# Optimization experiments

Measured on AMD Instinct MI355X. Metric: run time of the kernel, lower is better.

The kernel has to match this reference:

```python
import jax, jax.numpy as jnp
import numpy as np

B, S, D, H = 16, 512, 1024, 16
DH = D // H  # 64


def setup_inputs() -> dict:
    key = jax.random.key(0)
    kx, kq, kk, kv = jax.random.split(key, 4)
    stdv = 1.0 / np.sqrt(DH)  # reset_param uses 1/sqrt(t.size(1)) = 1/sqrt(head_dim)
    x = jax.random.normal(kx, (B, S, D), dtype=jnp.float32)
    Wq = jax.random.uniform(kq, (H, D, DH), dtype=jnp.float32, minval=-stdv, maxval=stdv)
    Wk = jax.random.uniform(kk, (H, D, DH), dtype=jnp.float32, minval=-stdv, maxval=stdv)
    Wv = jax.random.uniform(kv, (H, D, DH), dtype=jnp.float32, minval=-stdv, maxval=stdv)
    return {"x": x, "Wq": Wq, "Wk": Wk, "Wv": Wv}


def reference(x, Wq, Wk, Wv):
    # x: [B, S, D]; Wq/Wk/Wv: [H, D, DH] (stacked per-head params)
    q = jnp.einsum('bsd,hde->bhse', x, Wq)  # [B,H,S,DH]
    k = jnp.einsum('bsd,hde->bhse', x, Wk)
    v = jnp.einsum('bsd,hde->bhse', x, Wv)
    # NOTE: original scales by sqrt(input_dim), not sqrt(head_dim)
    scale = 1.0 / jnp.sqrt(jnp.float32(D))
    scores = jnp.einsum('bhse,bhte->bhst', q, k) * scale  # [B,H,S,S]
    attn = jax.nn.softmax(scores, axis=-1)
    out = jnp.einsum('bhst,bhte->bhse', attn, v)  # [B,H,S,DH]
    # concat heads along feature dim (head order matches torch cat over loop)
    return out.transpose(0, 2, 1, 3).reshape(x.shape[0], x.shape[1], D)
```

## Files before the change

kernel.cpp:

```cpp
#include <hip/hip_runtime.h>
#include <math.h>

constexpr int B = 16, S = 512, D = 1024, H = 16, DH = 64;
constexpr int BH = B * H;

typedef short bf16x8 __attribute__((ext_vector_type(8)));
typedef float f32x4  __attribute__((ext_vector_type(4)));

__device__ __forceinline__ unsigned short f2bf(float f) {
    unsigned u = __float_as_uint(f);
    u += 0x7fff + ((u >> 16) & 1);
    return (unsigned short)(u >> 16);
}

#define VMC0  asm volatile("s_waitcnt vmcnt(0)" ::: "memory")
#define BARR  __builtin_amdgcn_s_barrier()

__global__ __launch_bounds__(256) void convert_x(
    const float* __restrict__ x, unsigned short* __restrict__ xb)
{
    int i = blockIdx.x * 256 + threadIdx.x;
    float4 v = ((const float4*)x)[i];
    ushort4 o;
    o.x = f2bf(v.x); o.y = f2bf(v.y); o.z = f2bf(v.z); o.w = f2bf(v.w);
    ((ushort4*)xb)[i] = o;
}

__global__ __launch_bounds__(256) void convert_w(
    const float* __restrict__ Wq, const float* __restrict__ Wk,
    const float* __restrict__ Wv, unsigned short* __restrict__ WbT)
{
    __shared__ float tile[64][65];
    const int d0 = blockIdx.x * 64;
    const int h = blockIdx.y, m = blockIdx.z;
    const float* W = ((m == 0) ? Wq : (m == 1) ? Wk : Wv) + (size_t)h * D * DH;
    const int t = threadIdx.x;
    {
        int e = t & 63, dr = t >> 6;
        #pragma unroll
        for (int i = 0; i < 16; ++i) {
            int d = dr * 16 + i;
            tile[d][e] = W[(size_t)(d0 + d) * DH + e];
        }
    }
    __syncthreads();
    {
        int d = t & 63, er = t >> 6;
        unsigned short* out = WbT + (size_t)(m * H + h) * DH * D;
        #pragma unroll
        for (int i = 0; i < 16; ++i) {
            int e = er * 16 + i;
            out[(size_t)e * D + d0 + d] = f2bf(tile[d][e]);
        }
    }
}

__global__ __launch_bounds__(256) void qkv_gemm(
    const unsigned short* __restrict__ xb,
    const unsigned short* __restrict__ WbT,
    unsigned short* __restrict__ qkvb)
{
    __shared__ unsigned short As[128 * 64];
    __shared__ unsigned short Bs[128 * 64];

    const int t = threadIdx.x;
    const int w = t >> 6;
    const int wr = w >> 1, wc = w & 1;
    const int L = t & 63;
    const int lane15 = L & 15;
    const int quad = L >> 4;
    const int lrow8 = L >> 3;
    const int lg = L & 7;

    const int r0 = blockIdx.x * 128;
    const int n0 = blockIdx.y * 128;

    f32x4 acc[4][4] = {};

    for (int k0 = 0; k0 < D; k0 += 64) {
        #pragma unroll
        for (int i = 0; i < 4; ++i) {
            int c = w * 4 + i;
            int r = c * 8 + lrow8;
            int gg = lg ^ (r & 7);
            const unsigned short* gp = xb + (size_t)(r0 + r) * D + k0 + gg * 8;
            __builtin_amdgcn_global_load_lds(
                (const __attribute__((address_space(1))) void*)gp,
                (__attribute__((address_space(3))) void*)(As + c * 512),
                16, 0, 0);
            const unsigned short* gq = WbT + (size_t)(n0 + r) * D + k0 + gg * 8;
            __builtin_amdgcn_global_load_lds(
                (const __attribute__((address_space(1))) void*)gq,
                (__attribute__((address_space(3))) void*)(Bs + c * 512),
                16, 0, 0);
        }
        __syncthreads();

        #pragma unroll
        for (int ks = 0; ks < 2; ++ks) {
            int gk = ks * 4 + quad;
            bf16x8 a[4], bb[4];
            #pragma unroll
            for (int rt = 0; rt < 4; ++rt) {
                int ml = wr * 64 + rt * 16 + lane15;
                a[rt] = *(const bf16x8*)(As + ml * 64 + ((gk ^ (ml & 7)) * 8));
            }
            #pragma unroll
            for (int ct = 0; ct < 4; ++ct) {
                int nl = wc * 64 + ct * 16 + lane15;
                bb[ct] = *(const bf16x8*)(Bs + nl * 64 + ((gk ^ (nl & 7)) * 8));
            }
            #pragma unroll
            for (int rt = 0; rt < 4; ++rt)
                #pragma unroll
                for (int ct = 0; ct < 4; ++ct)
                    acc[rt][ct] = __builtin_amdgcn_mfma_f32_16x16x32_bf16(
                        a[rt], bb[ct], acc[rt][ct], 0, 0, 0);
        }
        __syncthreads();
    }

    const int m  = n0 >> 10;
    const int h  = ((n0 >> 6) + wc) & 15;
    const int bb_ = r0 >> 9;
    const int s0 = (r0 & 511) + wr * 64;

    if (m == 2) {
        unsigned short* outv = qkvb + ((size_t)(2 * BH) + (bb_ * H + h)) * (size_t)(S * DH);
        #pragma unroll
        for (int rt = 0; rt < 4; ++rt) {
            int srow = s0 + rt * 16 + quad * 4;
            #pragma unroll
            for (int ct = 0; ct < 4; ++ct) {
                int e = ct * 16 + lane15;
                ushort4 pk;
                pk.x = f2bf(acc[rt][ct][0]);
                pk.y = f2bf(acc[rt][ct][1]);
                pk.z = f2bf(acc[rt][ct][2]);
                pk.w = f2bf(acc[rt][ct][3]);
                *(ushort4*)(outv + (size_t)e * S + srow) = pk;
            }
        }
    } else {
        const float sc = (m == 0) ? 0.04508422002778011f : 1.0f;
        unsigned short* eb = (w < 2) ? (As + w * 4096) : (Bs + (w - 2) * 4096);
        #pragma unroll
        for (int rt = 0; rt < 4; ++rt)
            #pragma unroll
            for (int ct = 0; ct < 4; ++ct) {
                int e = ct * 16 + lane15;
                #pragma unroll
                for (int r = 0; r < 4; ++r) {
                    int row = rt * 16 + quad * 4 + r;
                    eb[row * 64 + (((e >> 3) ^ (row & 7)) * 8) + (e & 7)] =
                        f2bf(acc[rt][ct][r] * sc);
                }
            }
        unsigned short* outq = qkvb + ((size_t)m * BH + (bb_ * H + h)) * (size_t)(S * DH);
        #pragma unroll
        for (int j = 0; j < 8; ++j) {
            int row = j * 8 + lrow8;
            bf16x8 vv = *(const bf16x8*)(eb + row * 64 + ((lg ^ (row & 7)) * 8));
            *(bf16x8*)(outq + (size_t)(s0 + row) * DH + lg * 8) = vv;
        }
    }
}

__device__ __forceinline__ void stage_kv(
    const unsigned short* __restrict__ kb, const unsigned short* __restrict__ vt,
    int kt, unsigned short* Kd, unsigned short* Vd, int w, int lrow8, int lg)
{
    #pragma unroll
    for (int i = 0; i < 2; ++i) {
        int base = (w * 2 + i) * 8;
        int r = base + lrow8;
        int gr = (r & 32) | ((r & 12) << 1) | ((r & 16) >> 2) | (r & 3);
        int gg = lg ^ (r & 7);
        __builtin_amdgcn_global_load_lds(
            (const __attribute__((address_space(1))) void*)
                (kb + (size_t)(kt + gr) * DH + gg * 8),
            (__attribute__((address_space(3))) void*)(Kd + base * 64),
            16, 0, 0);
        __builtin_amdgcn_global_load_lds(
            (const __attribute__((address_space(1))) void*)
                (vt + (size_t)r * S + kt + gg * 8),
            (__attribute__((address_space(3))) void*)(Vd + base * 64),
            16, 0, 0);
    }
}

__global__ __launch_bounds__(256) void attn_mfma(
    const unsigned short* __restrict__ qkvb, float* __restrict__ out)
{
    __shared__ unsigned short Qs[128 * 64];
    __shared__ unsigned short Ks[2][64 * 64];
    __shared__ unsigned short Vt[2][64 * 64];

    const int t = threadIdx.x;
    const int w = t >> 6;
    const int L = t & 63;
    const int lane15 = L & 15;
    const int quad = L >> 4;
    const int lrow8 = L >> 3;
    const int lg = L & 7;
    const int qr0 = blockIdx.x * 128;
    const int bh = blockIdx.y;
    const int b = bh >> 4, h = bh & 15;

    const unsigned short* qb = qkvb + (size_t)bh * S * DH;
    const unsigned short* kb = qkvb + (size_t)(BH + bh) * S * DH;
    const unsigned short* vt = qkvb + (size_t)(2 * BH + bh) * S * DH;

    #pragma unroll
    for (int i = 0; i < 4; ++i) {
        int base = w * 32 + i * 8;
        int r = base + lrow8;
        int gg = lg ^ (r & 7);
        const unsigned short* gp = qb + (size_t)(qr0 + r) * DH + gg * 8;
        __builtin_amdgcn_global_load_lds(
            (const __attribute__((address_space(1))) void*)gp,
            (__attribute__((address_space(3))) void*)(Qs + base * 64),
            16, 0, 0);
    }
    stage_kv(kb, vt, 0, &Ks[0][0], &Vt[0][0], w, lrow8, lg);
    VMC0;
    BARR;

    bf16x8 qf[2][2];
    #pragma unroll
    for (int mt = 0; mt < 2; ++mt)
        #pragma unroll
        for (int ks = 0; ks < 2; ++ks) {
            int ml = w * 32 + mt * 16 + lane15;
            int gk = ks * 4 + quad;
            qf[mt][ks] = *(const bf16x8*)(Qs + ml * 64 + ((gk ^ (lane15 & 7)) * 8));
        }

    f32x4 o[2][4] = {};
    float plsum[2] = {0.f, 0.f};

    #pragma unroll 2
    for (int kt = 0; kt < S; kt += 64) {
        const int cur = (kt >> 6) & 1;
        const int nxt = cur ^ 1;

        bf16x8 kf[2][4], vf[2][4];
        #pragma unroll
        for (int ks = 0; ks < 2; ++ks) {
            int gk = ks * 4 + quad;
            #pragma unroll
            for (int ct = 0; ct < 4; ++ct) {
                int kr = ct * 16 + lane15;
                kf[ks][ct] = *(const bf16x8*)(&Ks[cur][0] + kr * 64 + ((gk ^ (lane15 & 7)) * 8));
                vf[ks][ct] = *(const bf16x8*)(&Vt[cur][0] + kr * 64 + ((gk ^ (lane15 & 7)) * 8));
            }
        }
        __builtin_amdgcn_sched_barrier(0);

        if (kt + 64 < S)
            stage_kv(kb, vt, kt + 64, &Ks[nxt][0], &Vt[nxt][0], w, lrow8, lg);

        f32x4 st[2][4] = {};
        __builtin_amdgcn_s_setprio(1);
        #pragma unroll
        for (int ks = 0; ks < 2; ++ks)
            #pragma unroll
            for (int mt = 0; mt < 2; ++mt)
                #pragma unroll
                for (int ct = 0; ct < 4; ++ct)
                    st[mt][ct] = __builtin_amdgcn_mfma_f32_16x16x32_bf16(
                        kf[ks][ct], qf[mt][ks], st[mt][ct], 0, 0, 0);
        __builtin_amdgcn_s_setprio(0);

        bf16x8 pB[2][2];
        #pragma unroll
        for (int mt = 0; mt < 2; ++mt) {
            float rs = 0.f;
            union { unsigned u[4]; bf16x8 v; } pu[2];
            #pragma unroll
            for (int ct = 0; ct < 4; ++ct) {
                float p0 = exp2f(st[mt][ct][0]);
                float p1 = exp2f(st[mt][ct][1]);
                float p2 = exp2f(st[mt][ct][2]);
                float p3 = exp2f(st[mt][ct][3]);
                rs += (p0 + p1) + (p2 + p3);
                unsigned lo, hi;
                asm("v_cvt_pk_bf16_f32 %0, %1, %2" : "=v"(lo) : "v"(p0), "v"(p1));
                asm("v_cvt_pk_bf16_f32 %0, %1, %2" : "=v"(hi) : "v"(p2), "v"(p3));
                pu[ct >> 1].u[(ct & 1) * 2 + 0] = lo;
                pu[ct >> 1].u[(ct & 1) * 2 + 1] = hi;
            }
            pB[mt][0] = pu[0].v;
            pB[mt][1] = pu[1].v;
            plsum[mt] += rs;
        }

        __builtin_amdgcn_s_setprio(1);
        #pragma unroll
        for (int ks = 0; ks < 2; ++ks)
            #pragma unroll
            for (int mt = 0; mt < 2; ++mt)
                #pragma unroll
                for (int nt = 0; nt < 4; ++nt)
                    o[mt][nt] = __builtin_amdgcn_mfma_f32_16x16x32_bf16(
                        vf[ks][nt], pB[mt][ks], o[mt][nt], 0, 0, 0);
        __builtin_amdgcn_s_setprio(0);

        VMC0;
        BARR;
    }

    #pragma unroll
    for (int mt = 0; mt < 2; ++mt) {
        float l = plsum[mt];
        l += __shfl_xor(l, 16, 64);
        l += __shfl_xor(l, 32, 64);
        float inv = 1.0f / l;
        int srow = qr0 + w * 32 + mt * 16 + lane15;
        float* op = out + (size_t)(b * S + srow) * D + h * DH;
        #pragma unroll
        for (int nt = 0; nt < 4; ++nt) {
            float4 v;
            v.x = o[mt][nt][0] * inv;
            v.y = o[mt][nt][1] * inv;
            v.z = o[mt][nt][2] * inv;
            v.w = o[mt][nt][3] * inv;
            *(float4*)(op + nt * 16 + quad * 4) = v;
        }
    }
}

extern "C" void kernel_launch(void* const* d_in, const int* in_sizes, int n_in,
                              void* d_out, int out_size, void* d_ws, size_t ws_size,
                              hipStream_t stream) {
    const float* x  = (const float*)d_in[0];
    const float* Wq = (const float*)d_in[1];
    const float* Wk = (const float*)d_in[2];
    const float* Wv = (const float*)d_in[3];
    float* outp = (float*)d_out;

    unsigned short* qkvb = (unsigned short*)d_ws;
    unsigned short* xb   = (unsigned short*)((char*)d_ws + 50331648);
    unsigned short* WbT  = (unsigned short*)((char*)d_ws + 67108864);

    convert_x<<<dim3((B * S * D / 4) / 256), 256, 0, stream>>>(x, xb);
    convert_w<<<dim3(D / 64, H, 3), 256, 0, stream>>>(Wq, Wk, Wv, WbT);
    qkv_gemm<<<dim3(B * S / 128, 3 * H * DH / 128), 256, 0, stream>>>(xb, WbT, qkvb);
    attn_mfma<<<dim3(S / 128, BH), 256, 0, stream>>>(qkvb, outp);
}
```

Before: 193.0 us.

## Load K/V fragments directly from global memory and drop LDS staging

The attention kernel no longer double-buffers K and V tiles in shared memory through global_load_lds with per-iteration barriers. Each lane now reads its MFMA fragments for K and transposed V straight from global memory, relying on L1/L2 caching. The QKV projection epilogue for Q and K likewise writes scattered 2-byte stores to global memory instead of staging through swizzled LDS for 16-byte coalesced stores. This removes barriers and LDS traffic, but exposes global load latency inside the loop and makes the projection stores uncoalesced.

```diff
diff --git a/kernel.cpp b/kernel.cpp
--- a/kernel.cpp
+++ b/kernel.cpp
@@ -143,49 +143,19 @@
         }
     } else {
         const float sc = (m == 0) ? 0.04508422002778011f : 1.0f;
-        unsigned short* eb = (w < 2) ? (As + w * 4096) : (Bs + (w - 2) * 4096);
-        #pragma unroll
-        for (int rt = 0; rt < 4; ++rt)
+        unsigned short* out = qkvb + ((size_t)m * BH + (bb_ * H + h)) * (size_t)(S * DH);
+        #pragma unroll
+        for (int rt = 0; rt < 4; ++rt) {
             #pragma unroll
             for (int ct = 0; ct < 4; ++ct) {
                 int e = ct * 16 + lane15;
                 #pragma unroll
                 for (int r = 0; r < 4; ++r) {
-                    int row = rt * 16 + quad * 4 + r;
-                    eb[row * 64 + (((e >> 3) ^ (row & 7)) * 8) + (e & 7)] =
-                        f2bf(acc[rt][ct][r] * sc);
+                    int srow = s0 + rt * 16 + quad * 4 + r;
+                    out[(size_t)srow * DH + e] = f2bf(acc[rt][ct][r] * sc);
                 }
             }
-        unsigned short* outq = qkvb + ((size_t)m * BH + (bb_ * H + h)) * (size_t)(S * DH);
-        #pragma unroll
-        for (int j = 0; j < 8; ++j) {
-            int row = j * 8 + lrow8;
-            bf16x8 vv = *(const bf16x8*)(eb + row * 64 + ((lg ^ (row & 7)) * 8));
-            *(bf16x8*)(outq + (size_t)(s0 + row) * DH + lg * 8) = vv;
-        }
-    }
-}
-
-__device__ __forceinline__ void stage_kv(
-    const unsigned short* __restrict__ kb, const unsigned short* __restrict__ vt,
-    int kt, unsigned short* Kd, unsigned short* Vd, int w, int lrow8, int lg)
-{
-    #pragma unroll
-    for (int i = 0; i < 2; ++i) {
-        int base = (w * 2 + i) * 8;
-        int r = base + lrow8;
-        int gr = (r & 32) | ((r & 12) << 1) | ((r & 16) >> 2) | (r & 3);
-        int gg = lg ^ (r & 7);
-        __builtin_amdgcn_global_load_lds(
-            (const __attribute__((address_space(1))) void*)
-                (kb + (size_t)(kt + gr) * DH + gg * 8),
-            (__attribute__((address_space(3))) void*)(Kd + base * 64),
-            16, 0, 0);
-        __builtin_amdgcn_global_load_lds(
-            (const __attribute__((address_space(1))) void*)
-                (vt + (size_t)r * S + kt + gg * 8),
-            (__attribute__((address_space(3))) void*)(Vd + base * 64),
-            16, 0, 0);
+        }
     }
 }
 
@@ -193,8 +163,6 @@
     const unsigned short* __restrict__ qkvb, float* __restrict__ out)
 {
     __shared__ unsigned short Qs[128 * 64];
-    __shared__ unsigned short Ks[2][64 * 64];
-    __shared__ unsigned short Vt[2][64 * 64];
 
     const int t = threadIdx.x;
     const int w = t >> 6;
@@ -222,7 +190,6 @@
             (__attribute__((address_space(3))) void*)(Qs + base * 64),
             16, 0, 0);
     }
-    stage_kv(kb, vt, 0, &Ks[0][0], &Vt[0][0], w, lrow8, lg);
     VMC0;
     BARR;
 
@@ -236,29 +203,24 @@
             qf[mt][ks] = *(const bf16x8*)(Qs + ml * 64 + ((gk ^ (lane15 & 7)) * 8));
         }
 
+    const int gl = (lane15 >> 2) * 8 + (lane15 & 3);
+    const unsigned short* kpl = kb + (size_t)gl * DH + quad * 8;
+    const unsigned short* vpl = vt + (size_t)lane15 * S + quad * 8;
+
     f32x4 o[2][4] = {};
     float plsum[2] = {0.f, 0.f};
 
     #pragma unroll 2
     for (int kt = 0; kt < S; kt += 64) {
-        const int cur = (kt >> 6) & 1;
-        const int nxt = cur ^ 1;
-
         bf16x8 kf[2][4], vf[2][4];
         #pragma unroll
-        for (int ks = 0; ks < 2; ++ks) {
-            int gk = ks * 4 + quad;
-            #pragma unroll
-            for (int ct = 0; ct < 4; ++ct) {
-                int kr = ct * 16 + lane15;
-                kf[ks][ct] = *(const bf16x8*)(&Ks[cur][0] + kr * 64 + ((gk ^ (lane15 & 7)) * 8));
-                vf[ks][ct] = *(const bf16x8*)(&Vt[cur][0] + kr * 64 + ((gk ^ (lane15 & 7)) * 8));
-            }
-        }
-        __builtin_amdgcn_sched_barrier(0);
-
-        if (kt + 64 < S)
-            stage_kv(kb, vt, kt + 64, &Ks[nxt][0], &Vt[nxt][0], w, lrow8, lg);
+        for (int ks = 0; ks < 2; ++ks)
+            #pragma unroll
+            for (int ct = 0; ct < 4; ++ct) {
+                int krow = kt + (ct >> 1) * 32 + (ct & 1) * 4;
+                kf[ks][ct] = *(const bf16x8*)(kpl + (size_t)krow * DH + ks * 32);
+                vf[ks][ct] = *(const bf16x8*)(vpl + (size_t)ct * (16 * S) + kt + ks * 32);
+            }
 
         f32x4 st[2][4] = {};
         __builtin_amdgcn_s_setprio(1);
@@ -305,9 +267,6 @@
                     o[mt][nt] = __builtin_amdgcn_mfma_f32_16x16x32_bf16(
                         vf[ks][nt], pB[mt][ks], o[mt][nt], 0, 0, 0);
         __builtin_amdgcn_s_setprio(0);
-
-        VMC0;
-        BARR;
     }
 
     #pragma unroll
```

Result: slower. 220.8 us (+14.4%).
